# Performance work log

Hardware: AMD Instinct MI355X
Metric: run time of the kernel (lower is better)

The kernel has to match this reference:

```python
import jax, jax.numpy as jnp
import numpy as np

L, C, H, W = 5, 16, 256, 256
DISCRETE_RATIO, DOWNSAMPLE_RATE = 0.4, 2
BN_EPS = 1e-5


def setup_inputs() -> dict:
    key = jax.random.key(0)
    ks = jax.random.split(key, 12)
    x = jax.random.normal(ks[0], (L, C, H, W), jnp.float32)
    # pairwise SE(2)-in-SE(3) transforms: small rotation about z + translation (meters)
    ang = jax.random.uniform(ks[1], (L, L), minval=-0.2, maxval=0.2)
    tx = jax.random.uniform(ks[2], (L, L), minval=-8.0, maxval=8.0)
    ty = jax.random.uniform(ks[3], (L, L), minval=-8.0, maxval=8.0)
    c, s = jnp.cos(ang), jnp.sin(ang)
    z, o = jnp.zeros_like(c), jnp.ones_like(c)
    ptm = jnp.stack([c, -s, z, tx,
                     s, c, z, ty,
                     z, z, o, z,
                     z, z, z, o], axis=-1).reshape(1, L, L, 4, 4).astype(jnp.float32)
    record_len = jnp.array([L], jnp.int32)

    def conv(k, o_, i_):
        k1, k2 = jax.random.split(k)
        w = jax.random.normal(k1, (o_, i_), jnp.float32) * np.float32(1.0 / np.sqrt(i_))
        b = jax.random.normal(k2, (o_,), jnp.float32) * 0.01
        return w, b

    def bn(k, n):
        k1, k2, k3, k4 = jax.random.split(k, 4)
        return (1.0 + 0.1 * jax.random.normal(k1, (n,), jnp.float32),
                0.1 * jax.random.normal(k2, (n,), jnp.float32),
                0.1 * jax.random.normal(k3, (n,), jnp.float32),
                1.0 + 0.1 * jax.random.uniform(k4, (n,), jnp.float32))

    w1, b1 = conv(ks[4], 16, 2 * C)
    g1, be1, rm1, rv1 = bn(ks[5], 16)
    w2, b2 = conv(ks[6], 8, 16)
    g2, be2, rm2, rv2 = bn(ks[7], 8)
    w3, b3 = conv(ks[8], 4, 8)
    g3, be3, rm3, rv3 = bn(ks[9], 4)
    w4, b4 = conv(ks[10], 1, 4)
    wm, bm = conv(ks[11], C, C)
    return dict(x=x, record_len=record_len, pairwise_t_matrix=ptm,
                w1=w1, b1=b1, g1=g1, be1=be1, rm1=rm1, rv1=rv1,
                w2=w2, b2=b2, g2=g2, be2=be2, rm2=rm2, rv2=rv2,
                w3=w3, b3=b3, g3=g3, be3=be3, rm3=rm3, rv3=rv3,
                w4=w4, b4=b4, wm=wm, bm=bm)


def _forward(x, pairwise_t_matrix, w1, b1, g1, be1, rm1, rv1,
             w2, b2, g2, be2, rm2, rv2, w3, b3, g3, be3, rm3, rv3,
             w4, b4, wm, bm):
    # get_discretized_transformation_matrix: rows [0,1], cols [0,1,3];
    # translation scaled by 1/(discrete_ratio*downsample_rate)
    m = pairwise_t_matrix.reshape(-1, L, 4, 4)
    T = jnp.concatenate([m[..., :2, :2],
                         m[..., :2, 3:4] / (DISCRETE_RATIO * DOWNSAMPLE_RATE)], axis=-1)
    T = T.reshape(1, L, L, 2, 3)[0]  # (J, I, 2, 3); T[j,i] warps agent j into frame i

    ys, xs = jnp.meshgrid(jnp.arange(H, dtype=jnp.float32),
                          jnp.arange(W, dtype=jnp.float32), indexing='ij')
    pts = jnp.stack([xs.ravel(), ys.ravel(), jnp.ones(H * W, jnp.float32)], 0)  # (3, HW)
    bottom = jnp.array([[0.0, 0.0, 1.0]], jnp.float32)

    def warp_one(img, M23):
        # normalize_homography + inverse + affine_grid(align_corners=True) collapses
        # to sampling src at inv(homog(M)) @ dst_pixel; grid_sample bilinear, zeros pad
        Minv = jnp.linalg.inv(jnp.concatenate([M23, bottom], 0))
        sxy = Minv[:2] @ pts  # (2, HW)
        sx, sy = sxy[0], sxy[1]
        x0, y0 = jnp.floor(sx), jnp.floor(sy)
        wx1, wy1 = sx - x0, sy - y0

        def tap(xi, yi, w):
            valid = (xi >= 0) & (xi <= W - 1) & (yi >= 0) & (yi <= H - 1)
            v = img[:, jnp.clip(yi, 0, H - 1).astype(jnp.int32),
                    jnp.clip(xi, 0, W - 1).astype(jnp.int32)]  # (C, HW)
            return v * jnp.where(valid, w, 0.0)[None]

        out = (tap(x0, y0, (1 - wx1) * (1 - wy1)) + tap(x0 + 1, y0, wx1 * (1 - wy1))
               + tap(x0, y0 + 1, (1 - wx1) * wy1) + tap(x0 + 1, y0 + 1, wx1 * wy1))
        return out.reshape(-1, H, W)

    # warp every agent j into every ego frame i: (J, I, C, H, W)
    warped = jax.vmap(lambda img, Mrow: jax.vmap(lambda M: warp_one(img, M))(Mrow))(x, T)
    nb = jnp.swapaxes(warped, 0, 1)                      # (I, J, C, H, W)
    ego = jnp.broadcast_to(x[:, None], (L, L, C, H, W))  # (I, J, C, H, W)
    f = jnp.concatenate([nb, ego], axis=2)               # (I, J, 2C, H, W)

    def cbr(f, w, b, g, be, rm, rv):
        y = jnp.einsum('ijchw,oc->ijohw', f, w) + b[:, None, None]
        y = (y - rm[:, None, None]) * (g[:, None, None] / jnp.sqrt(rv[:, None, None] + BN_EPS)) + be[:, None, None]
        return jax.nn.relu(y)

    f = cbr(f, w1, b1, g1, be1, rm1, rv1)
    f = cbr(f, w2, b2, g2, be2, rm2, rv2)
    f = cbr(f, w3, b3, g3, be3, rm3, rv3)
    f = jax.nn.relu(jnp.einsum('ijchw,oc->ijohw', f, w4) + b4[:, None, None])  # (I, J, 1, H, W)
    wgt = jax.nn.softmax(f, axis=1)  # softmax over neighbor (agent) axis == torch dim 0
    fused = jnp.sum(wgt * nb, axis=1)  # (I, C, H, W)
    return jnp.einsum('ichw,oc->iohw', fused, wm) + bm[:, None, None]


def reference(x, record_len, pairwise_t_matrix, w1, b1, g1, be1, rm1, rv1,
              w2, b2, g2, be2, rm2, rv2, w3, b3, g3, be3, rm3, rv3,
              w4, b4, wm, bm):
    # record_len is constant = L for B=1 (all agents present)
    del record_len
    return _forward(x, pairwise_t_matrix, w1, b1, g1, be1, rm1, rv1,
                    w2, b2, g2, be2, rm2, rv2, w3, b3, g3, be3, rm3, rv3,
                    w4, b4, wm, bm)
```

## Files before the change

kernel.cpp:

```cpp
#include <hip/hip_runtime.h>
#include <hip/hip_bf16.h>

typedef __hip_bfloat16 bf16;

#define L_AG 5
#define C_CH 16
#define H_SZ 256
#define W_SZ 256
#define HW_SZ (H_SZ * W_SZ)

__device__ __forceinline__ float ldf(const float* p) { return *p; }
__device__ __forceinline__ float ldf(const bf16* p)  { return __bfloat162float(*p); }
__device__ __forceinline__ void  stf(float* p, float v) { *p = v; }
__device__ __forceinline__ void  stf(bf16* p, float v)  { *p = __float2bfloat16(v); }

__global__ void dtype_detect(const unsigned short* __restrict__ xw, int* __restrict__ flag) {
    __shared__ int cnt;
    if (threadIdx.x == 0) cnt = 0;
    __syncthreads();
    int h = 0;
    for (int t = threadIdx.x; t < 512; t += 256) {
        const unsigned short w = xw[2 * t];
        const int e = (w >> 7) & 0xFF;
        h += (e >= 0x90) ? 1 : 0;
    }
    atomicAdd(&cnt, h);
    __syncthreads();
    if (threadIdx.x == 0) flag[0] = (cnt >= 16) ? 1 : 0;
}

__device__ __forceinline__ void tap_params(
    const float (*minv)[6], int j, float px, float py,
    int& po0, int& po1, float& aw0, float& bw0, float& aw1, float& bw1)
{
    const float m0 = minv[j][0], m1 = minv[j][1], m2 = minv[j][2];
    const float m3 = minv[j][3], m4 = minv[j][4], m5 = minv[j][5];
    const float sx = m0 * px + m1 * py + m2;
    const float sy = m3 * px + m4 * py + m5;
    const float fx0 = floorf(sx), fy0 = floorf(sy);
    const int x0 = (int)fx0, y0 = (int)fy0;
    const float wx1 = sx - fx0, wy1 = sy - fy0;
    const float wx0 = 1.0f - wx1, wy0 = 1.0f - wy1;
    const bool vx0 = (x0 >= 0) && (x0 <= W_SZ - 1);
    const bool vx1 = (x0 + 1 >= 0) && (x0 + 1 <= W_SZ - 1);
    const bool vy0 = (y0 >= 0) && (y0 <= H_SZ - 1);
    const bool vy1 = (y0 + 1 >= 0) && (y0 + 1 <= H_SZ - 1);
    const float w00 = (vx0 && vy0) ? wx0 * wy0 : 0.0f;
    const float w01 = (vx1 && vy0) ? wx1 * wy0 : 0.0f;
    const float w10 = (vx0 && vy1) ? wx0 * wy1 : 0.0f;
    const float w11 = (vx1 && vy1) ? wx1 * wy1 : 0.0f;
    const int cx0 = min(max(x0, 0), W_SZ - 1);
    const int cx1 = min(max(x0 + 1, 0), W_SZ - 1);
    const int cy0 = min(max(y0, 0), H_SZ - 1);
    const int cy1 = min(max(y0 + 1, 0), H_SZ - 1);
    const int cx0p = min(cx0, W_SZ - 2);
    const bool l0 = (cx0 == cx0p);
    const bool l1 = (cx1 == cx0p);
    aw0 = (l0 ? w00 : 0.0f) + (l1 ? w01 : 0.0f);
    bw0 = (l0 ? 0.0f : w00) + (l1 ? 0.0f : w01);
    aw1 = (l0 ? w10 : 0.0f) + (l1 ? w11 : 0.0f);
    bw1 = (l0 ? 0.0f : w10) + (l1 ? 0.0f : w11);
    po0 = cy0 * W_SZ + cx0p;
    po1 = cy1 * W_SZ + cx0p;
}

template <typename T, typename OT>
__global__ __launch_bounds__(256, 3) void disconet_fused(
    const T* __restrict__ x, const T* __restrict__ ptm,
    const T* __restrict__ w1, const T* __restrict__ b1,
    const T* __restrict__ g1, const T* __restrict__ be1,
    const T* __restrict__ rm1, const T* __restrict__ rv1,
    const T* __restrict__ w2, const T* __restrict__ b2,
    const T* __restrict__ g2, const T* __restrict__ be2,
    const T* __restrict__ rm2, const T* __restrict__ rv2,
    const T* __restrict__ w3, const T* __restrict__ b3,
    const T* __restrict__ g3, const T* __restrict__ be3,
    const T* __restrict__ rm3, const T* __restrict__ rv3,
    const T* __restrict__ w4, const T* __restrict__ b4,
    const T* __restrict__ wm, const T* __restrict__ bm,
    OT* __restrict__ out, const int* __restrict__ flag, const int want)
{
    if (flag[0] != want) return;

    __shared__ __align__(16) float s_w1[16 * 32];
    __shared__ float s_b1[16];
    __shared__ __align__(16) float s_w2[8 * 16];
    __shared__ float s_b2[8];
    __shared__ __align__(16) float s_w3[4 * 8];
    __shared__ float s_b3[4];
    __shared__ __align__(16) float s_w4v[4];
    __shared__ float s_b4;
    __shared__ __align__(16) float s_wm[16 * 16];
    __shared__ float s_bm[16];
    __shared__ float s_minv[L_AG][6];

    const int tid = threadIdx.x;

    const int bid      = blockIdx.x;
    const int tile_col = bid & 7;
    const int bp       = bid >> 3;
    const int i        = bp % L_AG;
    const int tile_row = bp / L_AG;

    const int px_i = (tile_col << 5) + (tid & 31);
    const int py_i = (tile_row << 3) + (tid >> 5);
    const int p    = py_i * W_SZ + px_i;

    for (int t = tid; t < 16 * 32; t += 256) {
        const int o = t >> 5;
        const float s = ldf(g1 + o) * rsqrtf(ldf(rv1 + o) + 1e-5f);
        s_w1[t] = ldf(w1 + t) * s;
    }
    if (tid < 128) {
        const int o = tid >> 4;
        const float s = ldf(g2 + o) * rsqrtf(ldf(rv2 + o) + 1e-5f);
        s_w2[tid] = ldf(w2 + tid) * s;
    }
    if (tid < 32) {
        const int o = tid >> 3;
        const float s = ldf(g3 + o) * rsqrtf(ldf(rv3 + o) + 1e-5f);
        s_w3[tid] = ldf(w3 + tid) * s;
    }
    if (tid < 16) {
        const float s1 = ldf(g1 + tid) * rsqrtf(ldf(rv1 + tid) + 1e-5f);
        s_b1[tid] = (ldf(b1 + tid) - ldf(rm1 + tid)) * s1 + ldf(be1 + tid);
        s_bm[tid] = ldf(bm + tid);
    }
    if (tid < 8) {
        const float s2 = ldf(g2 + tid) * rsqrtf(ldf(rv2 + tid) + 1e-5f);
        s_b2[tid] = (ldf(b2 + tid) - ldf(rm2 + tid)) * s2 + ldf(be2 + tid);
    }
    if (tid < 4) {
        const float s3 = ldf(g3 + tid) * rsqrtf(ldf(rv3 + tid) + 1e-5f);
        s_b3[tid] = (ldf(b3 + tid) - ldf(rm3 + tid)) * s3 + ldf(be3 + tid);
        s_w4v[tid] = ldf(w4 + tid);
    }
    if (tid == 0) s_b4 = ldf(b4);
    for (int t = tid; t < 256; t += 256) s_wm[t] = ldf(wm + t);

    if (tid < L_AG) {
        const int j = tid;
        const T* m = ptm + (j * L_AG + i) * 16;
        const float a  = ldf(m + 0);
        const float bb = ldf(m + 1);
        const float tx = ldf(m + 3) * 1.25f;
        const float c_ = ldf(m + 4);
        const float d  = ldf(m + 5);
        const float ty = ldf(m + 7) * 1.25f;
        float det = a * d - bb * c_;
        if (!(det > 1e-20f || det < -1e-20f)) det = 1.0f;
        const float invdet = 1.0f / det;
        s_minv[j][0] =  d * invdet;
        s_minv[j][1] = -bb * invdet;
        s_minv[j][2] = (bb * ty - d * tx) * invdet;
        s_minv[j][3] = -c_ * invdet;
        s_minv[j][4] =  a * invdet;
        s_minv[j][5] = (c_ * tx - a * ty) * invdet;
    }
    __syncthreads();

    const float px = (float)px_i;
    const float py = (float)py_i;

    float tl0[C_CH], th0[C_CH], tl1[C_CH], th1[C_CH];
    float caw0, cbw0, caw1, cbw1;

    {
        int po0, po1;
        tap_params(s_minv, 0, px, py, po0, po1, caw0, cbw0, caw1, cbw1);
#pragma unroll
        for (int c = 0; c < C_CH; ++c) {
            const T* ic = x + c * HW_SZ;
            tl0[c] = ldf(ic + po0); th0[c] = ldf(ic + po0 + 1);
            tl1[c] = ldf(ic + po1); th1[c] = ldf(ic + po1 + 1);
        }
    }

    float h1b[16];
    {
        float ego[C_CH];
        const T* xp = x + i * C_CH * HW_SZ + p;
#pragma unroll
        for (int c = 0; c < C_CH; ++c) ego[c] = ldf(xp + c * HW_SZ);
#pragma unroll
        for (int o = 0; o < 16; ++o) {
            float a = s_b1[o];
#pragma unroll
            for (int k = 0; k < 4; ++k) {
                const float4 w = *reinterpret_cast<const float4*>(&s_w1[o * 32 + 16 + 4 * k]);
                a += w.x * ego[4 * k] + w.y * ego[4 * k + 1] +
                     w.z * ego[4 * k + 2] + w.w * ego[4 * k + 3];
            }
            h1b[o] = a;
        }
    }

    float acc[C_CH];
#pragma unroll
    for (int c = 0; c < C_CH; ++c) acc[c] = 0.0f;
    float lsum = 0.0f;

#pragma unroll 1
    for (int j = 0; j < L_AG; ++j) {
        float nb[C_CH];
#pragma unroll
        for (int c = 0; c < C_CH; ++c)
            nb[c] = caw0 * tl0[c] + cbw0 * th0[c] +
                    caw1 * tl1[c] + cbw1 * th1[c];

        __builtin_amdgcn_sched_barrier(0);
        if (j + 1 < L_AG) {
            int po0, po1;
            tap_params(s_minv, j + 1, px, py, po0, po1, caw0, cbw0, caw1, cbw1);
            const T* img = x + (j + 1) * C_CH * HW_SZ;
#pragma unroll
            for (int c = 0; c < C_CH; ++c) {
                const T* ic = img + c * HW_SZ;
                tl0[c] = ldf(ic + po0); th0[c] = ldf(ic + po0 + 1);
                tl1[c] = ldf(ic + po1); th1[c] = ldf(ic + po1 + 1);
            }
        }
        __builtin_amdgcn_sched_barrier(0);

        float h1[16];
#pragma unroll
        for (int o = 0; o < 16; ++o) {
            float a = h1b[o];
#pragma unroll
            for (int k = 0; k < 4; ++k) {
                const float4 w = *reinterpret_cast<const float4*>(&s_w1[o * 32 + 4 * k]);
                a += w.x * nb[4 * k] + w.y * nb[4 * k + 1] +
                     w.z * nb[4 * k + 2] + w.w * nb[4 * k + 3];
            }
            h1[o] = fmaxf(a, 0.0f);
        }
        float h2[8];
#pragma unroll
        for (int o = 0; o < 8; ++o) {
            float a = s_b2[o];
#pragma unroll
            for (int k = 0; k < 4; ++k) {
                const float4 w = *reinterpret_cast<const float4*>(&s_w2[o * 16 + 4 * k]);
                a += w.x * h1[4 * k] + w.y * h1[4 * k + 1] +
                     w.z * h1[4 * k + 2] + w.w * h1[4 * k + 3];
            }
            h2[o] = fmaxf(a, 0.0f);
        }
        float h3[4];
#pragma unroll
        for (int o = 0; o < 4; ++o) {
            float a = s_b3[o];
#pragma unroll
            for (int k = 0; k < 2; ++k) {
                const float4 w = *reinterpret_cast<const float4*>(&s_w3[o * 8 + 4 * k]);
                a += w.x * h2[4 * k] + w.y * h2[4 * k + 1] +
                     w.z * h2[4 * k + 2] + w.w * h2[4 * k + 3];
            }
            h3[o] = fmaxf(a, 0.0f);
        }
        float sc = s_b4;
#pragma unroll
        for (int c = 0; c < 4; ++c) sc += s_w4v[c] * h3[c];
        sc = fminf(fmaxf(sc, 0.0f), 60.0f);

        const float es = __expf(sc);
        lsum += es;
#pragma unroll
        for (int c = 0; c < C_CH; ++c) acc[c] += es * nb[c];
    }

    const float invl = 1.0f / lsum;
#pragma unroll
    for (int c = 0; c < C_CH; ++c) acc[c] *= invl;

    OT* op = out + i * C_CH * HW_SZ + p;
#pragma unroll
    for (int o = 0; o < C_CH; ++o) {
        float a = s_bm[o];
#pragma unroll
        for (int k = 0; k < 4; ++k) {
            const float4 w = *reinterpret_cast<const float4*>(&s_wm[o * 16 + 4 * k]);
            a += w.x * acc[4 * k] + w.y * acc[4 * k + 1] +
                 w.z * acc[4 * k + 2] + w.w * acc[4 * k + 3];
        }
        stf(op + o * HW_SZ, a);
    }
}

extern "C" void kernel_launch(void* const* d_in, const int* in_sizes, int n_in,
                              void* d_out, int out_size, void* d_ws, size_t ws_size,
                              hipStream_t stream) {
    int* flag = (int*)d_ws;
    dtype_detect<<<1, 256, 0, stream>>>((const unsigned short*)d_in[0], flag);

    dim3 grid(8 * 32 * L_AG);

    disconet_fused<bf16, bf16><<<grid, 256, 0, stream>>>(
        (const bf16*)d_in[0], (const bf16*)d_in[2],
        (const bf16*)d_in[3], (const bf16*)d_in[4],
        (const bf16*)d_in[5], (const bf16*)d_in[6],
        (const bf16*)d_in[7], (const bf16*)d_in[8],
        (const bf16*)d_in[9], (const bf16*)d_in[10],
        (const bf16*)d_in[11], (const bf16*)d_in[12],
        (const bf16*)d_in[13], (const bf16*)d_in[14],
        (const bf16*)d_in[15], (const bf16*)d_in[16],
        (const bf16*)d_in[17], (const bf16*)d_in[18],
        (const bf16*)d_in[19], (const bf16*)d_in[20],
        (const bf16*)d_in[21], (const bf16*)d_in[22],
        (const bf16*)d_in[23], (const bf16*)d_in[24],
        (bf16*)d_out, flag, 0);

    disconet_fused<float, float><<<grid, 256, 0, stream>>>(
        (const float*)d_in[0], (const float*)d_in[2],
        (const float*)d_in[3], (const float*)d_in[4],
        (const float*)d_in[5], (const float*)d_in[6],
        (const float*)d_in[7], (const float*)d_in[8],
        (const float*)d_in[9], (const float*)d_in[10],
        (const float*)d_in[11], (const float*)d_in[12],
        (const float*)d_in[13], (const float*)d_in[14],
        (const float*)d_in[15], (const float*)d_in[16],
        (const float*)d_in[17], (const float*)d_in[18],
        (const float*)d_in[19], (const float*)d_in[20],
        (const float*)d_in[21], (const float*)d_in[22],
        (const float*)d_in[23], (const float*)d_in[24],
        (float*)d_out, flag, 1);
}
```

Before: 193.3 us.

## Use packed f32x2 FMAs for 1x1 convs and drop gather prefetch pipeline

Weights are transposed into shared memory as output-pair-packed f32x2 so each 1x1 conv layer runs as packed FMAs (v_pk_fma_f32) over broadcast inputs. The software prefetch of the next neighbor's bilinear taps is removed, so taps are now loaded inside the loop in two halves to lower register pressure. The occupancy hint in launch bounds is relaxed. The aim is to roughly halve the VALU instruction count of the MLP chain, at the cost of exposing gather latency that the prefetch used to hide.

```diff
diff --git a/kernel.cpp b/kernel.cpp
--- a/kernel.cpp
+++ b/kernel.cpp
@@ -2,6 +2,7 @@
 #include <hip/hip_bf16.h>
 
 typedef __hip_bfloat16 bf16;
+typedef float f32x2 __attribute__((ext_vector_type(2)));
 
 #define L_AG 5
 #define C_CH 16
@@ -13,6 +14,13 @@
 __device__ __forceinline__ float ldf(const bf16* p)  { return __bfloat162float(*p); }
 __device__ __forceinline__ void  stf(float* p, float v) { *p = v; }
 __device__ __forceinline__ void  stf(bf16* p, float v)  { *p = __float2bfloat16(v); }
+
+__device__ __forceinline__ f32x2 pk_fma(f32x2 a, f32x2 b, f32x2 c) {
+    return __builtin_elementwise_fma(a, b, c);
+}
+__device__ __forceinline__ f32x2 pk_relu(f32x2 a) {
+    return __builtin_elementwise_max(a, (f32x2){0.0f, 0.0f});
+}
 
 __global__ void dtype_detect(const unsigned short* __restrict__ xw, int* __restrict__ flag) {
     __shared__ int cnt;
@@ -65,7 +73,7 @@
 }
 
 template <typename T, typename OT>
-__global__ __launch_bounds__(256, 3) void disconet_fused(
+__global__ __launch_bounds__(256) void disconet_fused(
     const T* __restrict__ x, const T* __restrict__ ptm,
     const T* __restrict__ w1, const T* __restrict__ b1,
     const T* __restrict__ g1, const T* __restrict__ be1,
@@ -82,16 +90,16 @@
 {
     if (flag[0] != want) return;
 
-    __shared__ __align__(16) float s_w1[16 * 32];
-    __shared__ float s_b1[16];
-    __shared__ __align__(16) float s_w2[8 * 16];
-    __shared__ float s_b2[8];
-    __shared__ __align__(16) float s_w3[4 * 8];
-    __shared__ float s_b3[4];
+    __shared__ __align__(16) f32x2 s_w1p[32][8];
+    __shared__ __align__(16) float s_b1[16];
+    __shared__ __align__(16) f32x2 s_w2p[16][4];
+    __shared__ __align__(16) float s_b2[8];
+    __shared__ __align__(16) f32x2 s_w3p[8][2];
+    __shared__ __align__(16) float s_b3[4];
     __shared__ __align__(16) float s_w4v[4];
     __shared__ float s_b4;
-    __shared__ __align__(16) float s_wm[16 * 16];
-    __shared__ float s_bm[16];
+    __shared__ __align__(16) f32x2 s_wmp[16][8];
+    __shared__ __align__(16) float s_bm[16];
     __shared__ float s_minv[L_AG][6];
 
     const int tid = threadIdx.x;
@@ -106,20 +114,35 @@
     const int py_i = (tile_row << 3) + (tid >> 5);
     const int p    = py_i * W_SZ + px_i;
 
-    for (int t = tid; t < 16 * 32; t += 256) {
-        const int o = t >> 5;
-        const float s = ldf(g1 + o) * rsqrtf(ldf(rv1 + o) + 1e-5f);
-        s_w1[t] = ldf(w1 + t) * s;
-    }
-    if (tid < 128) {
-        const int o = tid >> 4;
-        const float s = ldf(g2 + o) * rsqrtf(ldf(rv2 + o) + 1e-5f);
-        s_w2[tid] = ldf(w2 + tid) * s;
-    }
-    if (tid < 32) {
-        const int o = tid >> 3;
-        const float s = ldf(g3 + o) * rsqrtf(ldf(rv3 + o) + 1e-5f);
-        s_w3[tid] = ldf(w3 + tid) * s;
+    {
+        const int cin = tid >> 3, o2 = tid & 7;
+        const int oa = 2 * o2, ob = 2 * o2 + 1;
+        const float sa = ldf(g1 + oa) * rsqrtf(ldf(rv1 + oa) + 1e-5f);
+        const float sb = ldf(g1 + ob) * rsqrtf(ldf(rv1 + ob) + 1e-5f);
+        s_w1p[cin][o2] = (f32x2){ ldf(w1 + oa * 32 + cin) * sa,
+                                  ldf(w1 + ob * 32 + cin) * sb };
+    }
+    if (tid < 64) {
+        const int cin = tid >> 2, o2 = tid & 3;
+        const int oa = 2 * o2, ob = 2 * o2 + 1;
+        const float sa = ldf(g2 + oa) * rsqrtf(ldf(rv2 + oa) + 1e-5f);
+        const float sb = ldf(g2 + ob) * rsqrtf(ldf(rv2 + ob) + 1e-5f);
+        s_w2p[cin][o2] = (f32x2){ ldf(w2 + oa * 16 + cin) * sa,
+                                  ldf(w2 + ob * 16 + cin) * sb };
+    }
+    if (tid < 16) {
+        const int cin = tid >> 1, o2 = tid & 1;
+        const int oa = 2 * o2, ob = 2 * o2 + 1;
+        const float sa = ldf(g3 + oa) * rsqrtf(ldf(rv3 + oa) + 1e-5f);
+        const float sb = ldf(g3 + ob) * rsqrtf(ldf(rv3 + ob) + 1e-5f);
+        s_w3p[cin][o2] = (f32x2){ ldf(w3 + oa * 8 + cin) * sa,
+                                  ldf(w3 + ob * 8 + cin) * sb };
+    }
+    if (tid >= 128 && tid < 256) {
+        const int t = tid - 128;
+        const int cin = t >> 3, o2 = t & 7;
+        s_wmp[cin][o2] = (f32x2){ ldf(wm + (2 * o2) * 16 + cin),
+                                  ldf(wm + (2 * o2 + 1) * 16 + cin) };
     }
     if (tid < 16) {
         const float s1 = ldf(g1 + tid) * rsqrtf(ldf(rv1 + tid) + 1e-5f);
@@ -136,7 +159,6 @@
         s_w4v[tid] = ldf(w4 + tid);
     }
     if (tid == 0) s_b4 = ldf(b4);
-    for (int t = tid; t < 256; t += 256) s_wm[t] = ldf(wm + t);
 
     if (tid < L_AG) {
         const int j = tid;
@@ -162,36 +184,19 @@
     const float px = (float)px_i;
     const float py = (float)py_i;
 
-    float tl0[C_CH], th0[C_CH], tl1[C_CH], th1[C_CH];
-    float caw0, cbw0, caw1, cbw1;
-
+    f32x2 h1bv[8];
+#pragma unroll
+    for (int o2 = 0; o2 < 8; ++o2)
+        h1bv[o2] = *reinterpret_cast<const f32x2*>(&s_b1[2 * o2]);
     {
-        int po0, po1;
-        tap_params(s_minv, 0, px, py, po0, po1, caw0, cbw0, caw1, cbw1);
+        const T* xp = x + i * C_CH * HW_SZ + p;
 #pragma unroll
         for (int c = 0; c < C_CH; ++c) {
-            const T* ic = x + c * HW_SZ;
-            tl0[c] = ldf(ic + po0); th0[c] = ldf(ic + po0 + 1);
-            tl1[c] = ldf(ic + po1); th1[c] = ldf(ic + po1 + 1);
-        }
-    }
-
-    float h1b[16];
-    {
-        float ego[C_CH];
-        const T* xp = x + i * C_CH * HW_SZ + p;
-#pragma unroll
-        for (int c = 0; c < C_CH; ++c) ego[c] = ldf(xp + c * HW_SZ);
-#pragma unroll
-        for (int o = 0; o < 16; ++o) {
-            float a = s_b1[o];
-#pragma unroll
-            for (int k = 0; k < 4; ++k) {
-                const float4 w = *reinterpret_cast<const float4*>(&s_w1[o * 32 + 16 + 4 * k]);
-                a += w.x * ego[4 * k] + w.y * ego[4 * k + 1] +
-                     w.z * ego[4 * k + 2] + w.w * ego[4 * k + 3];
-            }
-            h1b[o] = a;
+            const float e = ldf(xp + c * HW_SZ);
+            const f32x2 bc = (f32x2){e, e};
+#pragma unroll
+            for (int o2 = 0; o2 < 8; ++o2)
+                h1bv[o2] = pk_fma(s_w1p[16 + c][o2], bc, h1bv[o2]);
         }
     }
 
@@ -202,65 +207,77 @@
 
 #pragma unroll 1
     for (int j = 0; j < L_AG; ++j) {
+        int po0, po1;
+        float aw0, bw0, aw1, bw1;
+        tap_params(s_minv, j, px, py, po0, po1, aw0, bw0, aw1, bw1);
+        const T* img = x + j * C_CH * HW_SZ;
+
         float nb[C_CH];
-#pragma unroll
-        for (int c = 0; c < C_CH; ++c)
-            nb[c] = caw0 * tl0[c] + cbw0 * th0[c] +
-                    caw1 * tl1[c] + cbw1 * th1[c];
-
-        __builtin_amdgcn_sched_barrier(0);
-        if (j + 1 < L_AG) {
-            int po0, po1;
-            tap_params(s_minv, j + 1, px, py, po0, po1, caw0, cbw0, caw1, cbw1);
-            const T* img = x + (j + 1) * C_CH * HW_SZ;
+        {
+            float tl[C_CH], th[C_CH];
 #pragma unroll
             for (int c = 0; c < C_CH; ++c) {
                 const T* ic = img + c * HW_SZ;
-                tl0[c] = ldf(ic + po0); th0[c] = ldf(ic + po0 + 1);
-                tl1[c] = ldf(ic + po1); th1[c] = ldf(ic + po1 + 1);
+                tl[c] = ldf(ic + po0); th[c] = ldf(ic + po0 + 1);
             }
-        }
-        __builtin_amdgcn_sched_barrier(0);
-
-        float h1[16];
-#pragma unroll
-        for (int o = 0; o < 16; ++o) {
-            float a = h1b[o];
-#pragma unroll
-            for (int k = 0; k < 4; ++k) {
-                const float4 w = *reinterpret_cast<const float4*>(&s_w1[o * 32 + 4 * k]);
-                a += w.x * nb[4 * k] + w.y * nb[4 * k + 1] +
-                     w.z * nb[4 * k + 2] + w.w * nb[4 * k + 3];
+#pragma unroll
+            for (int c = 0; c < C_CH; ++c) nb[c] = aw0 * tl[c] + bw0 * th[c];
+        }
+        {
+            float tl[C_CH], th[C_CH];
+#pragma unroll
+            for (int c = 0; c < C_CH; ++c) {
+                const T* ic = img + c * HW_SZ;
+                tl[c] = ldf(ic + po1); th[c] = ldf(ic + po1 + 1);
             }
-            h1[o] = fmaxf(a, 0.0f);
-        }
-        float h2[8];
-#pragma unroll
-        for (int o = 0; o < 8; ++o) {
-            float a = s_b2[o];
-#pragma unroll
-            for (int k = 0; k < 4; ++k) {
-                const float4 w = *reinterpret_cast<const float4*>(&s_w2[o * 16 + 4 * k]);
-                a += w.x * h1[4 * k] + w.y * h1[4 * k + 1] +
-                     w.z * h1[4 * k + 2] + w.w * h1[4 * k + 3];
-            }
-            h2[o] = fmaxf(a, 0.0f);
-        }
-        float h3[4];
-#pragma unroll
-        for (int o = 0; o < 4; ++o) {
-            float a = s_b3[o];
-#pragma unroll
-            for (int k = 0; k < 2; ++k) {
-                const float4 w = *reinterpret_cast<const float4*>(&s_w3[o * 8 + 4 * k]);
-                a += w.x * h2[4 * k] + w.y * h2[4 * k + 1] +
-                     w.z * h2[4 * k + 2] + w.w * h2[4 * k + 3];
-            }
-            h3[o] = fmaxf(a, 0.0f);
-        }
-        float sc = s_b4;
-#pragma unroll
-        for (int c = 0; c < 4; ++c) sc += s_w4v[c] * h3[c];
+#pragma unroll
+            for (int c = 0; c < C_CH; ++c) nb[c] += aw1 * tl[c] + bw1 * th[c];
+        }
+
+        f32x2 h1v[8];
+#pragma unroll
+        for (int o2 = 0; o2 < 8; ++o2) h1v[o2] = h1bv[o2];
+#pragma unroll
+        for (int c = 0; c < C_CH; ++c) {
+            const f32x2 bc = (f32x2){nb[c], nb[c]};
+#pragma unroll
+            for (int o2 = 0; o2 < 8; ++o2)
+                h1v[o2] = pk_fma(s_w1p[c][o2], bc, h1v[o2]);
+        }
+#pragma unroll
+        for (int o2 = 0; o2 < 8; ++o2) h1v[o2] = pk_relu(h1v[o2]);
+
+        f32x2 h2v[4];
+#pragma unroll
+        for (int o2 = 0; o2 < 4; ++o2)
+            h2v[o2] = *reinterpret_cast<const f32x2*>(&s_b2[2 * o2]);
+#pragma unroll
+        for (int c = 0; c < 16; ++c) {
+            const float hs = (c & 1) ? h1v[c >> 1].y : h1v[c >> 1].x;
+            const f32x2 bc = (f32x2){hs, hs};
+#pragma unroll
+            for (int o2 = 0; o2 < 4; ++o2)
+                h2v[o2] = pk_fma(s_w2p[c][o2], bc, h2v[o2]);
+        }
+#pragma unroll
+        for (int o2 = 0; o2 < 4; ++o2) h2v[o2] = pk_relu(h2v[o2]);
+
+        f32x2 h3v[2];
+#pragma unroll
+        for (int o2 = 0; o2 < 2; ++o2)
+            h3v[o2] = *reinterpret_cast<const f32x2*>(&s_b3[2 * o2]);
+#pragma unroll
+        for (int c = 0; c < 8; ++c) {
+            const float hs = (c & 1) ? h2v[c >> 1].y : h2v[c >> 1].x;
+            const f32x2 bc = (f32x2){hs, hs};
+#pragma unroll
+            for (int o2 = 0; o2 < 2; ++o2)
+                h3v[o2] = pk_fma(s_w3p[c][o2], bc, h3v[o2]);
+        }
+        h3v[0] = pk_relu(h3v[0]); h3v[1] = pk_relu(h3v[1]);
+
+        float sc = s_b4 + s_w4v[0] * h3v[0].x + s_w4v[1] * h3v[0].y
+                        + s_w4v[2] * h3v[1].x + s_w4v[3] * h3v[1].y;
         sc = fminf(fmaxf(sc, 0.0f), 60.0f);
 
         const float es = __expf(sc);
@@ -273,17 +290,22 @@
 #pragma unroll
     for (int c = 0; c < C_CH; ++c) acc[c] *= invl;
 
+    f32x2 outv[8];
+#pragma unroll
+    for (int o2 = 0; o2 < 8; ++o2)
+        outv[o2] = *reinterpret_cast<const f32x2*>(&s_bm[2 * o2]);
+#pragma unroll
+    for (int c = 0; c < C_CH; ++c) {
+        const f32x2 bc = (f32x2){acc[c], acc[c]};
+#pragma unroll
+        for (int o2 = 0; o2 < 8; ++o2)
+            outv[o2] = pk_fma(s_wmp[c][o2], bc, outv[o2]);
+    }
     OT* op = out + i * C_CH * HW_SZ + p;
 #pragma unroll
-    for (int o = 0; o < C_CH; ++o) {
-        float a = s_bm[o];
-#pragma unroll
-        for (int k = 0; k < 4; ++k) {
-            const float4 w = *reinterpret_cast<const float4*>(&s_wm[o * 16 + 4 * k]);
-            a += w.x * acc[4 * k] + w.y * acc[4 * k + 1] +
-                 w.z * acc[4 * k + 2] + w.w * acc[4 * k + 3];
-        }
-        stf(op + o * HW_SZ, a);
+    for (int o2 = 0; o2 < 8; ++o2) {
+        stf(op + (2 * o2) * HW_SZ,     outv[o2].x);
+        stf(op + (2 * o2 + 1) * HW_SZ, outv[o2].y);
     }
 }
 
```

Result: slower. 251.5 us (+30.1%).
